# Optimization experiments

Hardware: AMD Instinct MI355X
Metric: run time of the kernel (lower is better)

## Reference

```python
import jax, jax.numpy as jnp
import numpy as np

ROPE_BASE = 10000.0


def _rope_cos_sin(n, d, dtype):
    # standard llama-style rotary embedding over head dim d
    inv_freq = 1.0 / (ROPE_BASE ** (jnp.arange(0, d, 2, dtype=jnp.float32) / d))
    t = jnp.arange(n, dtype=jnp.float32)
    freqs = jnp.einsum('n,f->nf', t, inv_freq)          # [N, d/2]
    emb = jnp.concatenate([freqs, freqs], axis=-1)      # [N, d]
    return jnp.cos(emb).astype(dtype), jnp.sin(emb).astype(dtype)


def _rotate_half(x):
    x1, x2 = jnp.split(x, 2, axis=-1)
    return jnp.concatenate([-x2, x1], axis=-1)


def _apply_rope(x, cos, sin):
    # x: [B, H, N, D]; cos/sin: [N, D] broadcast over B, H
    return x * cos + _rotate_half(x) * sin


def setup_inputs() -> dict:
    key = jax.random.key(0)
    k1, k2, k3 = jax.random.split(key, 3)
    B, N, dim = 2, 2048, 1024
    heads, dim_head = 16, 64
    inner = heads * dim_head
    x = jax.random.normal(k1, (B, N, dim), dtype=jnp.float32)
    w_qkv = jax.random.normal(k2, (dim, 3 * inner), dtype=jnp.float32) * (dim ** -0.5)
    w_out = jax.random.normal(k3, (inner, dim), dtype=jnp.float32) * (inner ** -0.5)
    return {"x": x, "w_qkv": w_qkv, "w_out": w_out}


def reference(x, w_qkv, w_out):
    B, N, _ = x.shape
    heads, dim_head = 16, 64
    qkv = jnp.einsum('bnd,de->bne', x, w_qkv)
    q, k, v = jnp.split(qkv, 3, axis=-1)
    def to_heads(t):
        return t.reshape(B, N, heads, dim_head).transpose(0, 2, 1, 3)  # [B,H,N,D]
    q, k, v = to_heads(q), to_heads(k), to_heads(v)
    cos, sin = _rope_cos_sin(N, dim_head, x.dtype)
    q = _apply_rope(q, cos, sin)
    k = _apply_rope(k, cos, sin)
    scale = dim_head ** -0.5
    scores = jnp.einsum('bhqd,bhkd->bhqk', q, k) * scale   # [B,H,N,N], non-causal
    attn = jax.nn.softmax(scores, axis=-1)
    out = jnp.einsum('bhqk,bhkd->bhqd', attn, v)
    out = out.transpose(0, 2, 1, 3).reshape(B, N, heads * dim_head)
    return jnp.einsum('bne,ed->bnd', out, w_out)
```

## Files before the change

### kernel.cpp

```cpp
#include <hip/hip_runtime.h>

typedef __attribute__((ext_vector_type(8))) short bf16x8;
typedef __attribute__((ext_vector_type(4))) float f32x4;

#define MFMA(a, b, c) __builtin_amdgcn_mfma_f32_16x16x32_bf16(a, b, c, 0, 0, 0)

__device__ __forceinline__ unsigned short f2bf(float f) {
    unsigned u = __builtin_bit_cast(unsigned, f);
    u += 0x7fffu + ((u >> 16) & 1u);
    return (unsigned short)(u >> 16);
}

__device__ __forceinline__ void gload16(const unsigned short* g, unsigned short* l) {
    __builtin_amdgcn_global_load_lds(
        (const __attribute__((address_space(1))) void*)g,
        (__attribute__((address_space(3))) void*)l, 16, 0, 0);
}

__device__ __forceinline__ unsigned pack_bf16(float lo, float hi) {
    unsigned a = __builtin_bit_cast(unsigned, lo) + 0x8000u;
    unsigned b = __builtin_bit_cast(unsigned, hi) + 0x8000u;
    return __builtin_amdgcn_perm(b, a, 0x07060302);
}


__global__ __launch_bounds__(256) void cvt_bf16(const float* __restrict__ in,
                                                unsigned short* __restrict__ out, int n) {
    int i = (blockIdx.x * 256 + threadIdx.x) * 4;
    if (i < n) {
        float4 f = *(const float4*)(in + i);
        ushort4 u;
        u.x = f2bf(f.x); u.y = f2bf(f.y); u.z = f2bf(f.z); u.w = f2bf(f.w);
        *(ushort4*)(out + i) = u;
    }
}

__global__ __launch_bounds__(256) void transpose_cvt(const float* __restrict__ in,
                                                     unsigned short* __restrict__ out,
                                                     int R, int C) {
    __shared__ float tile[32][33];
    const int c0 = blockIdx.x * 32, r0 = blockIdx.y * 32;
    const int tr = threadIdx.x >> 3;
    const int j4 = (threadIdx.x & 7) * 4;
    float4 f = *(const float4*)(in + (size_t)(r0 + tr) * C + c0 + j4);
    tile[tr][j4 + 0] = f.x; tile[tr][j4 + 1] = f.y;
    tile[tr][j4 + 2] = f.z; tile[tr][j4 + 3] = f.w;
    __syncthreads();
    ushort4 u;
    u.x = f2bf(tile[j4 + 0][tr]); u.y = f2bf(tile[j4 + 1][tr]);
    u.z = f2bf(tile[j4 + 2][tr]); u.w = f2bf(tile[j4 + 3][tr]);
    *(ushort4*)(out + (size_t)(c0 + tr) * R + r0 + j4) = u;
}

__global__ __launch_bounds__(256) void rope_tab(float* __restrict__ cosT,
                                                float* __restrict__ sinT) {
    int i = blockIdx.x * 256 + threadIdx.x;
    int n = i >> 5, f = i & 31;
    float ang = (float)n * exp2f((float)f * -0.4152410118609203f);
    float s, c;
    sincosf(ang, &s, &c);
    cosT[i] = c; sinT[i] = s;
}


#define PHASE(AB, BB, MH, NH, DOA, DOB)                                           \
    do {                                                                          \
        if (DOA) {                                                                \
            _Pragma("unroll") for (int mf = 0; mf < 4; mf++)                      \
                _Pragma("unroll") for (int kc = 0; kc < 2; kc++)                  \
                    af[mf][kc] = *(const bf16x8*)&(AB)[                           \
                        (wm * 128 + MH * 64 + mf * 16 + cc) * 64 +                \
                        ((kc * 4 + quad) ^ (cc & 7)) * 8];                        \
        }                                                                         \
        if (DOB) {                                                                \
            _Pragma("unroll") for (int nf = 0; nf < 2; nf++)                      \
                _Pragma("unroll") for (int kc = 0; kc < 2; kc++)                  \
                    bfr[nf][kc] = *(const bf16x8*)&(BB)[                          \
                        (wn * 64 + NH * 32 + nf * 16 + cc) * 64 +                 \
                        ((kc * 4 + quad) ^ (cc & 7)) * 8];                        \
        }                                                                         \
        __builtin_amdgcn_s_setprio(1);                                            \
        _Pragma("unroll") for (int mf = 0; mf < 4; mf++)                          \
            _Pragma("unroll") for (int nf = 0; nf < 2; nf++)                      \
                _Pragma("unroll") for (int kc = 0; kc < 2; kc++)                  \
                    acc[MH * 4 + mf][NH * 2 + nf] = MFMA(                         \
                        af[mf][kc], bfr[nf][kc], acc[MH * 4 + mf][NH * 2 + nf]);  \
        __builtin_amdgcn_s_setprio(0);                                            \
    } while (0)

__global__ __launch_bounds__(512, 2) void gemm_qkv(const unsigned short* __restrict__ A,
                                                   const unsigned short* __restrict__ Bt,
                                                   unsigned short* __restrict__ oq,
                                                   unsigned short* __restrict__ ok,
                                                   unsigned short* __restrict__ ovt,
                                                   const float* __restrict__ cosT,
                                                   const float* __restrict__ sinT) {
    __shared__ unsigned short Ab[2][256 * 64];
    __shared__ unsigned short Bb[2][256 * 64];
    const int tid = threadIdx.x;
    const int w = tid >> 6, lane = tid & 63, quad = lane >> 4, cc = lane & 15;
    const int wm = w >> 2, wn = w & 3;
    const int m0 = blockIdx.y * 256, n0 = blockIdx.x * 256;

    int soff[4], lb[4];
#pragma unroll
    for (int j = 0; j < 4; j++) {
        int S = j * 512 + w * 64 + lane;
        int row = S >> 3;
        int c = (S & 7) ^ (row & 7);
        soff[j] = row * 1024 + c * 8;
        lb[j] = (j * 512 + w * 64) * 8;
    }
    const unsigned short* Ag = A + (size_t)m0 * 1024;
    const unsigned short* Bg = Bt + (size_t)n0 * 1024;

    auto stage = [&](const unsigned short* g, unsigned short* l) {
#pragma unroll
        for (int j = 0; j < 4; j++) gload16(g + soff[j], l + lb[j]);
    };

    f32x4 acc[8][4] = {};
    bf16x8 af[4][2], bfr[2][2];

    stage(Ag, &Ab[0][0]);
    stage(Bg, &Bb[0][0]);
    asm volatile("s_waitcnt vmcnt(0)" ::: "memory");
    __builtin_amdgcn_s_barrier();

    for (int t = 0; t < 8; ++t) {
        const int k0 = 2 * t;
        stage(Ag + (k0 + 1) * 64, &Ab[1][0]);
        stage(Bg + (k0 + 1) * 64, &Bb[1][0]);
        PHASE(Ab[0], Bb[0], 0, 0, true, true);
        __builtin_amdgcn_s_barrier();
        PHASE(Ab[0], Bb[0], 0, 1, false, true);
        __builtin_amdgcn_s_barrier();
        PHASE(Ab[0], Bb[0], 1, 1, true, false);
        __builtin_amdgcn_s_barrier();
        PHASE(Ab[0], Bb[0], 1, 0, false, true);
        asm volatile("s_waitcnt vmcnt(0)" ::: "memory");
        __builtin_amdgcn_s_barrier();
        if (t < 7) {
            stage(Ag + (k0 + 2) * 64, &Ab[0][0]);
            stage(Bg + (k0 + 2) * 64, &Bb[0][0]);
        }
        PHASE(Ab[1], Bb[1], 0, 0, true, true);
        __builtin_amdgcn_s_barrier();
        PHASE(Ab[1], Bb[1], 0, 1, false, true);
        __builtin_amdgcn_s_barrier();
        PHASE(Ab[1], Bb[1], 1, 1, true, false);
        __builtin_amdgcn_s_barrier();
        PHASE(Ab[1], Bb[1], 1, 0, false, true);
        asm volatile("s_waitcnt vmcnt(0)" ::: "memory");
        __builtin_amdgcn_s_barrier();
    }

    const int e0 = n0 + wn * 64;
    const int which = e0 >> 10;
    const int h = (e0 >> 6) & 15;
    if (which < 2) {
        unsigned short* dst = (which == 0) ? oq : ok;
        const float postscale = (which == 0) ? 0.125f : 1.0f;
#pragma unroll
        for (int mf = 0; mf < 8; mf++) {
#pragma unroll
            for (int r = 0; r < 4; r++) {
                int mg = m0 + wm * 128 + mf * 16 + quad * 4 + r;
                int nseq = mg & 2047, b = mg >> 11;
                float vals[4];
#pragma unroll
                for (int nf = 0; nf < 4; nf++) vals[nf] = acc[mf][nf][r];
                size_t rowbase = ((size_t)(b * 16 + h) * 2048 + nseq) * 64;
#pragma unroll
                for (int nf = 0; nf < 4; nf++) {
                    int d = nf * 16 + cc;
                    int f = d & 31;
                    float cs = cosT[nseq * 32 + f];
                    float sn = sinT[nseq * 32 + f];
                    float partner = vals[nf ^ 2];
                    float outv = (vals[nf] * cs +
                                  ((nf < 2) ? -partner : partner) * sn) * postscale;
                    dst[rowbase + d] = f2bf(outv);
                }
            }
        }
    } else {
#pragma unroll
        for (int mf = 0; mf < 8; mf++) {
            int mg0 = m0 + wm * 128 + mf * 16 + quad * 4;
            int b = mg0 >> 11, nseq = mg0 & 2047;
#pragma unroll
            for (int nf = 0; nf < 4; nf++) {
                int d = nf * 16 + cc;
                ushort4 pk;
                pk.x = f2bf(acc[mf][nf][0]);
                pk.y = f2bf(acc[mf][nf][1]);
                pk.z = f2bf(acc[mf][nf][2]);
                pk.w = f2bf(acc[mf][nf][3]);
                *(ushort4*)(ovt + ((size_t)(b * 16 + h) * 64 + d) * 2048 + nseq) = pk;
            }
        }
    }
}


__global__ __launch_bounds__(256, 3) void gemm_out(const unsigned short* __restrict__ A,
                                                   const unsigned short* __restrict__ Bt,
                                                   int K, int Ncols,
                                                   float* __restrict__ of) {
    __shared__ unsigned short As[2][128 * 32];
    __shared__ unsigned short Bs[2][128 * 32];
    const int tid = threadIdx.x;
    const int w = tid >> 6, lane = tid & 63, quad = lane >> 4, cc = lane & 15;
    const int wm = w >> 1, wn = w & 1;
    const int m0 = blockIdx.y * 128, n0 = blockIdx.x * 128;

    size_t aoff[2], boff[2];
#pragma unroll
    for (int t = 0; t < 2; t++) {
        int S = w * 128 + t * 64 + lane;
        int row = S >> 2;
        int c = (S & 3) ^ ((row >> 1) & 3);
        aoff[t] = (size_t)(m0 + row) * K + c * 8;
        boff[t] = (size_t)(n0 + row) * K + c * 8;
    }

#pragma unroll
    for (int t = 0; t < 2; t++) {
        gload16(A + aoff[t], &As[0][(w * 2 + t) * 512]);
        gload16(Bt + boff[t], &Bs[0][(w * 2 + t) * 512]);
    }
    __syncthreads();

    f32x4 acc[4][4] = {};
    const int rpos = (quad ^ ((cc >> 1) & 3)) * 8;
    const int nkt = K >> 5;

    for (int kt = 0; kt < nkt; kt++) {
        const int pb = kt & 1;
        if (kt < nkt - 1) {
            const int ko = (kt + 1) * 32;
#pragma unroll
            for (int t = 0; t < 2; t++) {
                gload16(A + aoff[t] + ko, &As[pb ^ 1][(w * 2 + t) * 512]);
                gload16(Bt + boff[t] + ko, &Bs[pb ^ 1][(w * 2 + t) * 512]);
            }
        }
        bf16x8 afv[4], bfv[4];
#pragma unroll
        for (int i = 0; i < 4; i++)
            afv[i] = *(const bf16x8*)&As[pb][(wm * 64 + i * 16 + cc) * 32 + rpos];
#pragma unroll
        for (int i = 0; i < 4; i++)
            bfv[i] = *(const bf16x8*)&Bs[pb][(wn * 64 + i * 16 + cc) * 32 + rpos];
#pragma unroll
        for (int i = 0; i < 4; i++)
#pragma unroll
            for (int j = 0; j < 4; j++)
                acc[i][j] = MFMA(afv[i], bfv[j], acc[i][j]);
        __syncthreads();
    }

#pragma unroll
    for (int mf = 0; mf < 4; mf++)
#pragma unroll
        for (int nf = 0; nf < 4; nf++)
#pragma unroll
            for (int r = 0; r < 4; r++) {
                int mg = m0 + wm * 64 + mf * 16 + quad * 4 + r;
                of[(size_t)mg * Ncols + n0 + wn * 64 + nf * 16 + cc] = acc[mf][nf][r];
            }
}


__global__ __launch_bounds__(512, 4) void attn(const unsigned short* __restrict__ q,
                                               const unsigned short* __restrict__ k,
                                               const unsigned short* __restrict__ vt,
                                               unsigned short* __restrict__ o) {
    __shared__ unsigned short ks[2][64 * 64];
    __shared__ unsigned short vs[2][64 * 64];
    __shared__ unsigned short ps[128 * 72];
    __shared__ float rsb[128];
    const int tid = threadIdx.x;
    const int w = tid >> 6, lane = tid & 63, quad = lane >> 4, cc = lane & 15;
    const int bh = blockIdx.x & 31, qt = blockIdx.x >> 5;

    const unsigned short* qg = q + ((size_t)bh * 2048 + qt * 128 + w * 16) * 64;
    bf16x8 aq[2];
#pragma unroll
    for (int kc = 0; kc < 2; kc++)
        aq[kc] = *(const bf16x8*)(qg + cc * 64 + kc * 32 + quad * 8);

    const int S = w * 64 + lane;
    const int row = S >> 3;
    const int c = (S & 7) ^ (row & 7);
    const int koff = row * 64 + c * 8;
    const int voff = row * 2048 + c * 8;

    const unsigned short* kg0 = k + (size_t)bh * 2048 * 64;
    const unsigned short* vg0 = vt + (size_t)bh * 64 * 2048;

    gload16(kg0 + koff, &ks[0][w * 512]);
    gload16(vg0 + voff, &vs[0][w * 512]);
    __syncthreads();

    f32x4 oacc[4] = {};
    float rs = 0.f;

    for (int kt = 0; kt < 32; kt++) {
        const int pb = kt & 1;
        if (kt < 31) {
            const unsigned short* kb = kg0 + (kt + 1) * 4096;
            const unsigned short* vb = vg0 + (kt + 1) * 64;
            gload16(kb + koff, &ks[pb ^ 1][w * 512]);
            gload16(vb + voff, &vs[pb ^ 1][w * 512]);
        }

        f32x4 s2[4] = {};
        __builtin_amdgcn_s_setprio(1);
#pragma unroll
        for (int kc = 0; kc < 2; kc++) {
#pragma unroll
            for (int nf = 0; nf < 4; nf++) {
                bf16x8 bk = *(const bf16x8*)&ks[pb][(nf * 16 + cc) * 64 +
                                                    ((kc * 4 + quad) ^ (cc & 7)) * 8];
                s2[nf] = MFMA(bk, aq[kc], s2[nf]);
            }
        }
        __builtin_amdgcn_s_setprio(0);

#pragma unroll
        for (int nf = 0; nf < 4; nf++) {
            float p0 = __builtin_amdgcn_exp2f(
                __builtin_fmaf(s2[nf][0], 1.44269504f, -11.54156036f));
            float p1 = __builtin_amdgcn_exp2f(
                __builtin_fmaf(s2[nf][1], 1.44269504f, -11.54156036f));
            float p2 = __builtin_amdgcn_exp2f(
                __builtin_fmaf(s2[nf][2], 1.44269504f, -11.54156036f));
            float p3 = __builtin_amdgcn_exp2f(
                __builtin_fmaf(s2[nf][3], 1.44269504f, -11.54156036f));
            rs += (p0 + p1) + (p2 + p3);
            uint2 pk;
            pk.x = pack_bf16(p0, p1);
            pk.y = pack_bf16(p2, p3);
            *(uint2*)&ps[(w * 16 + cc) * 72 + nf * 16 + quad * 4] = pk;
        }

#pragma unroll
        for (int kc = 0; kc < 2; kc++) {
            bf16x8 ap = *(const bf16x8*)&ps[(w * 16 + cc) * 72 + kc * 32 + quad * 8];
            __builtin_amdgcn_s_setprio(1);
#pragma unroll
            for (int df = 0; df < 4; df++) {
                bf16x8 bv = *(const bf16x8*)&vs[pb][(df * 16 + cc) * 64 +
                                                    ((kc * 4 + quad) ^ (cc & 7)) * 8];
                oacc[df] = MFMA(ap, bv, oacc[df]);
            }
            __builtin_amdgcn_s_setprio(0);
        }

        __syncthreads();
    }

    rs += __shfl_xor(rs, 16, 64);
    rs += __shfl_xor(rs, 32, 64);
    if (quad == 0) rsb[w * 16 + cc] = rs;

    {
        f32x4 rv = *(const f32x4*)&rsb[w * 16 + quad * 4];
        f32x4 inv;
#pragma unroll
        for (int r = 0; r < 4; r++) inv[r] = 1.0f / rv[r];
#pragma unroll
        for (int r = 0; r < 4; r++)
#pragma unroll
            for (int df = 0; df < 4; df++)
                ps[(w * 16 + quad * 4 + r) * 72 + df * 16 + cc] =
                    f2bf(oacc[df][r] * inv[r]);
    }
    __syncthreads();
    {
        const int b = bh >> 4, h = bh & 15;
        int row2 = tid >> 2, seg = tid & 3;
        unsigned short* og =
            o + ((size_t)(b * 2048 + qt * 128 + row2)) * 1024 + h * 64 + seg * 16;
#pragma unroll
        for (int j = 0; j < 2; j++)
            *(uint4*)(og + j * 8) = *(const uint4*)&ps[row2 * 72 + seg * 16 + j * 8];
    }
}


extern "C" void kernel_launch(void* const* d_in, const int* in_sizes, int n_in,
                              void* d_out, int out_size, void* d_ws, size_t ws_size,
                              hipStream_t stream) {
    const float* x = (const float*)d_in[0];
    const float* w_qkv = (const float*)d_in[1];
    const float* w_out = (const float*)d_in[2];
    float* out = (float*)d_out;

    unsigned short* xb    = (unsigned short*)d_ws;
    unsigned short* wqkvT = xb + 4096 * 1024;
    unsigned short* woutT = wqkvT + 3072 * 1024;
    unsigned short* qb    = woutT + 1024 * 1024;
    unsigned short* kb    = qb + 2 * 16 * 2048 * 64;
    unsigned short* vtb   = kb + 2 * 16 * 2048 * 64;
    unsigned short* ob    = vtb + 2 * 16 * 2048 * 64;
    float* cosT = (float*)(ob + 4096 * 1024);
    float* sinT = cosT + 2048 * 32;

    rope_tab<<<256, 256, 0, stream>>>(cosT, sinT);
    cvt_bf16<<<4096, 256, 0, stream>>>(x, xb, 4096 * 1024);
    transpose_cvt<<<dim3(96, 32), 256, 0, stream>>>(w_qkv, wqkvT, 1024, 3072);
    transpose_cvt<<<dim3(32, 32), 256, 0, stream>>>(w_out, woutT, 1024, 1024);
    gemm_qkv<<<dim3(12, 16), 512, 0, stream>>>(xb, wqkvT, qb, kb, vtb, cosT, sinT);
    attn<<<512, 512, 0, stream>>>(qb, kb, vtb, ob);
    gemm_out<<<dim3(8, 32), 256, 0, stream>>>(ob, woutT, 1024, 1024, out);
}
```

Measured before the change: 191.0 us.

## Interleave quarter-tile global-to-LDS prefetches across GEMM phases with partial vmcnt waits

Restructures the QKV GEMM main loop so each of the four MFMA phases issues one quarter of the next K-tile's global-to-LDS loads, staged in the order the following phases consume them. A partial s_waitcnt vmcnt and a barrier now sit around every phase, replacing the single full drain per half-iteration. The aim is to spread memory traffic evenly across compute and avoid full vmcnt(0) stalls, at the cost of more barriers and tighter correctness dependence on the counter values and load ordering.

```diff
diff --git a/kernel.cpp b/kernel.cpp
--- a/kernel.cpp
+++ b/kernel.cpp
@@ -63,22 +63,24 @@
 }
 
 
-#define PHASE(AB, BB, MH, NH, DOA, DOB)                                           \
+#define PH(ABUF, BBUF, MH, NH, DOA, DOB, VMC, ...)                                \
     do {                                                                          \
         if (DOA) {                                                                \
             _Pragma("unroll") for (int mf = 0; mf < 4; mf++)                      \
                 _Pragma("unroll") for (int kc = 0; kc < 2; kc++)                  \
-                    af[mf][kc] = *(const bf16x8*)&(AB)[                           \
+                    af[mf][kc] = *(const bf16x8*)&(ABUF)[                         \
                         (wm * 128 + MH * 64 + mf * 16 + cc) * 64 +                \
                         ((kc * 4 + quad) ^ (cc & 7)) * 8];                        \
         }                                                                         \
         if (DOB) {                                                                \
             _Pragma("unroll") for (int nf = 0; nf < 2; nf++)                      \
                 _Pragma("unroll") for (int kc = 0; kc < 2; kc++)                  \
-                    bfr[nf][kc] = *(const bf16x8*)&(BB)[                          \
+                    bfr[nf][kc] = *(const bf16x8*)&(BBUF)[                        \
                         (wn * 64 + NH * 32 + nf * 16 + cc) * 64 +                 \
                         ((kc * 4 + quad) ^ (cc & 7)) * 8];                        \
         }                                                                         \
+        __VA_ARGS__;                                                              \
+        asm volatile("s_barrier" ::: "memory");                                   \
         __builtin_amdgcn_s_setprio(1);                                            \
         _Pragma("unroll") for (int mf = 0; mf < 4; mf++)                          \
             _Pragma("unroll") for (int nf = 0; nf < 2; nf++)                      \
@@ -86,7 +88,18 @@
                     acc[MH * 4 + mf][NH * 2 + nf] = MFMA(                         \
                         af[mf][kc], bfr[nf][kc], acc[MH * 4 + mf][NH * 2 + nf]);  \
         __builtin_amdgcn_s_setprio(0);                                            \
+        asm volatile("s_waitcnt vmcnt(" VMC ")" ::: "memory");                    \
+        asm volatile("s_barrier" ::: "memory");                                   \
     } while (0)
+
+#define STAGEA0(t1, buf) { gload16(Ag + gA00 + (t1) * 64, (buf) + lA00);          \
+                           gload16(Ag + gA01 + (t1) * 64, (buf) + lA01); }
+#define STAGEA1(t1, buf) { gload16(Ag + gA10 + (t1) * 64, (buf) + lA10);          \
+                           gload16(Ag + gA11 + (t1) * 64, (buf) + lA11); }
+#define STAGEB0(t1, buf) { gload16(Bg + gB00 + (t1) * 64, (buf) + lB00);          \
+                           gload16(Bg + gB01 + (t1) * 64, (buf) + lB01); }
+#define STAGEB1(t1, buf) { gload16(Bg + gB10 + (t1) * 64, (buf) + lB10);          \
+                           gload16(Bg + gB11 + (t1) * 64, (buf) + lB11); }
 
 __global__ __launch_bounds__(512, 2) void gemm_qkv(const unsigned short* __restrict__ A,
                                                    const unsigned short* __restrict__ Bt,
@@ -102,57 +115,54 @@
     const int wm = w >> 2, wn = w & 3;
     const int m0 = blockIdx.y * 256, n0 = blockIdx.x * 256;
 
-    int soff[4], lb[4];
-#pragma unroll
-    for (int j = 0; j < 4; j++) {
-        int S = j * 512 + w * 64 + lane;
-        int row = S >> 3;
-        int c = (S & 7) ^ (row & 7);
-        soff[j] = row * 1024 + c * 8;
-        lb[j] = (j * 512 + w * 64) * 8;
-    }
     const unsigned short* Ag = A + (size_t)m0 * 1024;
     const unsigned short* Bg = Bt + (size_t)n0 * 1024;
 
-    auto stage = [&](const unsigned short* g, unsigned short* l) {
-#pragma unroll
-        for (int j = 0; j < 4; j++) gload16(g + soff[j], l + lb[j]);
-    };
+    int gA00, gA01, gA10, gA11, lA00, lA01, lA10, lA11;
+    int gB00, gB01, gB10, gB11, lB00, lB01, lB10, lB11;
+#define MKA(mh, j, G, L)                                                \
+    { int S = (wm * 128 + mh * 64) * 8 + j * 256 + wn * 64 + lane;      \
+      int r = S >> 3; int c = (S & 7) ^ (r & 7);                        \
+      G = r * 1024 + c * 8; L = (S - lane) * 8; }
+#define MKB(nh, j, G, L)                                                \
+    { int S = (wn * 64 + nh * 32) * 8 + j * 128 + wm * 64 + lane;       \
+      int r = S >> 3; int c = (S & 7) ^ (r & 7);                        \
+      G = r * 1024 + c * 8; L = (S - lane) * 8; }
+    MKA(0, 0, gA00, lA00) MKA(0, 1, gA01, lA01)
+    MKA(1, 0, gA10, lA10) MKA(1, 1, gA11, lA11)
+    MKB(0, 0, gB00, lB00) MKB(0, 1, gB01, lB01)
+    MKB(1, 0, gB10, lB10) MKB(1, 1, gB11, lB11)
+#undef MKA
+#undef MKB
 
     f32x4 acc[8][4] = {};
     bf16x8 af[4][2], bfr[2][2];
 
-    stage(Ag, &Ab[0][0]);
-    stage(Bg, &Bb[0][0]);
-    asm volatile("s_waitcnt vmcnt(0)" ::: "memory");
-    __builtin_amdgcn_s_barrier();
-
-    for (int t = 0; t < 8; ++t) {
-        const int k0 = 2 * t;
-        stage(Ag + (k0 + 1) * 64, &Ab[1][0]);
-        stage(Bg + (k0 + 1) * 64, &Bb[1][0]);
-        PHASE(Ab[0], Bb[0], 0, 0, true, true);
-        __builtin_amdgcn_s_barrier();
-        PHASE(Ab[0], Bb[0], 0, 1, false, true);
-        __builtin_amdgcn_s_barrier();
-        PHASE(Ab[0], Bb[0], 1, 1, true, false);
-        __builtin_amdgcn_s_barrier();
-        PHASE(Ab[0], Bb[0], 1, 0, false, true);
-        asm volatile("s_waitcnt vmcnt(0)" ::: "memory");
-        __builtin_amdgcn_s_barrier();
-        if (t < 7) {
-            stage(Ag + (k0 + 2) * 64, &Ab[0][0]);
-            stage(Bg + (k0 + 2) * 64, &Bb[0][0]);
-        }
-        PHASE(Ab[1], Bb[1], 0, 0, true, true);
-        __builtin_amdgcn_s_barrier();
-        PHASE(Ab[1], Bb[1], 0, 1, false, true);
-        __builtin_amdgcn_s_barrier();
-        PHASE(Ab[1], Bb[1], 1, 1, true, false);
-        __builtin_amdgcn_s_barrier();
-        PHASE(Ab[1], Bb[1], 1, 0, false, true);
-        asm volatile("s_waitcnt vmcnt(0)" ::: "memory");
-        __builtin_amdgcn_s_barrier();
+    STAGEA0(0, &Ab[0][0]);
+    STAGEB0(0, &Bb[0][0]);
+    STAGEB1(0, &Bb[0][0]);
+    STAGEA1(0, &Ab[0][0]);
+    asm volatile("s_waitcnt vmcnt(4)" ::: "memory");
+    asm volatile("s_barrier" ::: "memory");
+
+    for (int t = 0; t < 15; ++t) {
+        const unsigned short* Ac = &Ab[t & 1][0];
+        const unsigned short* Bc = &Bb[t & 1][0];
+        unsigned short* An = &Ab[(t + 1) & 1][0];
+        unsigned short* Bn = &Bb[(t + 1) & 1][0];
+        const int t1 = t + 1;
+        PH(Ac, Bc, 0, 0, true, true, "4", STAGEA0(t1, An));
+        PH(Ac, Bc, 0, 1, false, true, "4", STAGEB0(t1, Bn));
+        PH(Ac, Bc, 1, 1, true, false, "4", STAGEB1(t1, Bn));
+        PH(Ac, Bc, 1, 0, false, true, "4", STAGEA1(t1, An));
+    }
+    {
+        const unsigned short* Ac = &Ab[1][0];
+        const unsigned short* Bc = &Bb[1][0];
+        PH(Ac, Bc, 0, 0, true, true, "2", );
+        PH(Ac, Bc, 0, 1, false, true, "0", );
+        PH(Ac, Bc, 1, 1, true, false, "0", );
+        PH(Ac, Bc, 1, 0, false, true, "0", );
     }
 
     const int e0 = n0 + wn * 64;
```

Measured after the change: 190.7 us. No clear change (-0.1%).
